# Kernel optimization log

Hardware: AMD Instinct MI355X
Metric: run time of the kernel (lower is better)

## Reference

```python
import jax, jax.numpy as jnp
import numpy as np

DIM = 128
POS_HID = 32
ATTN_HID = 2 * DIM
K = 16
B, N = 4, 4096


def setup_inputs() -> dict:
    key = jax.random.key(0)
    ks = jax.random.split(key, 16)
    s = lambda fan_in: 1.0 / np.sqrt(fan_in)
    inp = {
        "x": jax.random.normal(ks[0], (B, N, DIM), dtype=jnp.float32),
        "pos": jax.random.uniform(ks[1], (B, N, 3), dtype=jnp.float32),
        # linear projections (stored as (in, out); y = x @ W)
        "Wq": jax.random.uniform(ks[2], (DIM, DIM), minval=-s(DIM), maxval=s(DIM)),
        "Wk": jax.random.uniform(ks[3], (DIM, DIM), minval=-s(DIM), maxval=s(DIM)),
        "Wv": jax.random.uniform(ks[4], (DIM, DIM), minval=-s(DIM), maxval=s(DIM)),
        # pos_mlp: 3 -> POS_HID -> DIM
        "p_w1": jax.random.uniform(ks[5], (3, POS_HID), minval=-s(3), maxval=s(3)),
        "p_b1": jax.random.uniform(ks[6], (POS_HID,), minval=-s(3), maxval=s(3)),
        "p_w2": jax.random.uniform(ks[7], (POS_HID, DIM), minval=-s(POS_HID), maxval=s(POS_HID)),
        "p_b2": jax.random.uniform(ks[8], (DIM,), minval=-s(POS_HID), maxval=s(POS_HID)),
        # attn_mlp: DIM -> ATTN_HID -> DIM
        "a_w1": jax.random.uniform(ks[9], (DIM, ATTN_HID), minval=-s(DIM), maxval=s(DIM)),
        "a_b1": jax.random.uniform(ks[10], (ATTN_HID,), minval=-s(DIM), maxval=s(DIM)),
        "a_w2": jax.random.uniform(ks[11], (ATTN_HID, DIM), minval=-s(ATTN_HID), maxval=s(ATTN_HID)),
        "a_b2": jax.random.uniform(ks[12], (DIM,), minval=-s(ATTN_HID), maxval=s(ATTN_HID)),
    }
    return inp


def reference(x, pos, Wq, Wk, Wv, p_w1, p_b1, p_w2, p_b2, a_w1, a_b1, a_w2, a_b2):
    # brute-force kNN: (B, N, N) squared distances, take K smallest
    dists = jnp.sum((pos[:, :, None, :] - pos[:, None, :, :]) ** 2, axis=-1)
    _, knn_idx = jax.lax.top_k(-dists, K)                      # (B, N, K)

    gather = jax.vmap(lambda tbl, idx: tbl[idx])               # (N, C)[ (N,K) ] -> (N,K,C)
    knn_xyz = gather(pos, knn_idx)                              # (B, N, K, 3)

    q = x @ Wq                                                  # (B, N, D)
    k = gather(x @ Wk, knn_idx)                                 # (B, N, K, D)
    v = gather(x @ Wv, knn_idx)                                 # (B, N, K, D)

    rel = pos[:, :, None, :] - knn_xyz                          # (B, N, K, 3)
    pos_enc = jax.nn.relu(rel @ p_w1 + p_b1) @ p_w2 + p_b2      # (B, N, K, D)

    h = q[:, :, None, :] - k + pos_enc                          # (B, N, K, D)
    attn = jax.nn.relu(h @ a_w1 + a_b1) @ a_w2 + a_b2           # (B, N, K, D)
    attn = jax.nn.softmax(attn / np.sqrt(DIM), axis=-2)         # softmax over K

    agg = jnp.einsum("bnkd,bnkd->bnd", attn, v + pos_enc)       # (B, N, D)
    return agg
```

## Files before the change

### kernel.cpp

```cpp
#include <hip/hip_runtime.h>
#include <hip/hip_bf16.h>

#define B_   4
#define N_   4096
#define D_   128
#define PH_  32
#define AH_  256
#define K_   16
#define BN_  (B_*N_)

#define S2_  16
#define SC2_ (N_ / S2_)

typedef __attribute__((ext_vector_type(8))) short short8;
typedef __attribute__((ext_vector_type(4))) float f32x4;

__device__ inline float f4c(const float4& v, int i) {
  return i == 0 ? v.x : i == 1 ? v.y : i == 2 ? v.z : v.w;
}

__device__ inline unsigned short f2bf(float f) {
  unsigned u = __float_as_uint(f);
  unsigned r = u + 0x7fffu + ((u >> 16) & 1u);
  return (unsigned short)(r >> 16);
}

__device__ inline unsigned short f2bfn(float f) {
  __hip_bfloat16 h = __float2bfloat16(f);
  return *reinterpret_cast<unsigned short*>(&h);
}

__device__ inline float bf2f(unsigned short u) {
  return __uint_as_float((unsigned)u << 16);
}

__global__ __launch_bounds__(256) void wshuf_kernel(
    const float* __restrict__ a_w1, const float* __restrict__ a_w2,
    const float* __restrict__ p_w2,
    const float* __restrict__ Wq, const float* __restrict__ Wk, const float* __restrict__ Wv,
    unsigned short* __restrict__ W1f, unsigned short* __restrict__ W2f,
    unsigned short* __restrict__ p2f,
    unsigned short* __restrict__ Wqf, unsigned short* __restrict__ Wkf,
    unsigned short* __restrict__ Wvf)
{
  int tid = blockIdx.x * blockDim.x + threadIdx.x;
  for (int f = tid; f < 4096; f += blockDim.x * gridDim.x) {
    int lane = f & 63, g = lane >> 4, c = lane & 15;
    {
      int nt = f >> 8, kc = (f >> 6) & 3;
      unsigned short o[8];
      #pragma unroll
      for (int j = 0; j < 8; ++j)
        o[j] = f2bf(a_w1[(size_t)(32 * kc + 8 * g + j) * 256 + 16 * nt + c]);
      #pragma unroll
      for (int j = 0; j < 8; ++j) W1f[(size_t)f * 8 + j] = o[j];
    }
    {
      int nt = f >> 9, kc = (f >> 6) & 7;
      unsigned short o[8];
      #pragma unroll
      for (int j = 0; j < 8; ++j)
        o[j] = f2bf(a_w2[(size_t)(32 * kc + 8 * g + j) * 128 + 16 * nt + c]);
      #pragma unroll
      for (int j = 0; j < 8; ++j) W2f[(size_t)f * 8 + j] = o[j];
    }
    if (f < 512) {
      int nt = f >> 6;
      unsigned short o[8];
      #pragma unroll
      for (int j = 0; j < 8; ++j)
        o[j] = f2bf(p_w2[(size_t)(8 * g + j) * 128 + 16 * nt + c]);
      #pragma unroll
      for (int j = 0; j < 8; ++j) p2f[(size_t)f * 8 + j] = o[j];
    }
    if (f < 2048) {
      int nt = f >> 8, kc = (f >> 6) & 3;
      unsigned short oq[8], ok[8], ov[8];
      #pragma unroll
      for (int j = 0; j < 8; ++j) {
        size_t src = (size_t)(32 * kc + 8 * g + j) * 128 + 16 * nt + c;
        oq[j] = f2bf(Wq[src]);
        ok[j] = f2bf(Wk[src]);
        ov[j] = f2bf(Wv[src]);
      }
      #pragma unroll
      for (int j = 0; j < 8; ++j) {
        Wqf[(size_t)f * 8 + j] = oq[j];
        Wkf[(size_t)f * 8 + j] = ok[j];
        Wvf[(size_t)f * 8 + j] = ov[j];
      }
    }
  }
}

__global__ __launch_bounds__(256) void qkv_mfma_kernel(
    const float* __restrict__ x,
    const unsigned short* __restrict__ Wqf, const unsigned short* __restrict__ Wkf,
    const unsigned short* __restrict__ Wvf,
    float* __restrict__ xq, float* __restrict__ xk, float* __restrict__ xv)
{
  const int w = threadIdx.x >> 6, lane = threadIdx.x & 63;
  const int g = lane >> 4, c = lane & 15;
  const int r0 = (blockIdx.x * 4 + w) * 16;

  short8 xa[4];
  const float* xrow = x + (size_t)(r0 + c) * 128;
  #pragma unroll
  for (int kc = 0; kc < 4; ++kc) {
    const int d0 = 32 * kc + 8 * g;
    float4 a4 = *(const float4*)(xrow + d0);
    float4 b4 = *(const float4*)(xrow + d0 + 4);
    #pragma unroll
    for (int j = 0; j < 8; ++j) {
      float vv = j < 4 ? f4c(a4, j) : f4c(b4, j - 4);
      xa[kc][j] = (short)f2bfn(vv);
    }
  }

  const unsigned short* Ws[3] = {Wqf, Wkf, Wvf};
  float* outs[3] = {xq, xk, xv};
  const f32x4 zero4 = {0.f, 0.f, 0.f, 0.f};

  #pragma unroll
  for (int m = 0; m < 3; ++m) {
    f32x4 acc[8];
    #pragma unroll
    for (int i = 0; i < 8; ++i) acc[i] = zero4;
    #pragma unroll
    for (int nt = 0; nt < 8; ++nt) {
      #pragma unroll
      for (int kc = 0; kc < 4; ++kc) {
        short8 bf = *(const short8*)(Ws[m] + ((size_t)(nt * 4 + kc) * 64 + lane) * 8);
        acc[nt] = __builtin_amdgcn_mfma_f32_16x16x32_bf16(xa[kc], bf, acc[nt], 0, 0, 0);
      }
    }
    #pragma unroll
    for (int nt = 0; nt < 8; ++nt)
      #pragma unroll
      for (int r = 0; r < 4; ++r)
        outs[m][(size_t)(r0 + 4 * g + r) * 128 + nt * 16 + c] = acc[nt][r];
  }
}

__global__ __launch_bounds__(256) void knn_sel_kernel(const float* __restrict__ pos,
                                                      float* __restrict__ part)
{
  __shared__ float4 sh[SC2_];
  const int tid = threadIdx.x;
  const int q = blockIdx.x * 256 + tid;
  const int sp = blockIdx.y;
  const int b = q >> 12, i = q & (N_ - 1);
  const float* __restrict__ pb = pos + (size_t)b * N_ * 3;
  const int j0 = sp * SC2_;

  for (int e = tid; e < SC2_; e += 256) {
    const float* src = pb + (size_t)(j0 + e) * 3;
    sh[e] = make_float4(src[0], src[1], src[2], 0.f);
  }
  const float qx = pb[i * 3 + 0], qy = pb[i * 3 + 1], qz = pb[i * 3 + 2];
  __syncthreads();

  float c[16];
  #pragma unroll
  for (int s = 0; s < 16; ++s) c[s] = __int_as_float(0x7f800000);

  #pragma unroll 4
  for (int j = 0; j < SC2_; ++j) {
    float4 pt = sh[j];
    float dx = qx - pt.x;
    float dy = qy - pt.y;
    float dz = qz - pt.z;
    float d2 = __fadd_rn(__fadd_rn(__fmul_rn(dx, dx), __fmul_rn(dy, dy)), __fmul_rn(dz, dz));
    #pragma unroll
    for (int s = 15; s >= 1; --s) c[s] = __builtin_amdgcn_fmed3f(c[s - 1], c[s], d2);
    c[0] = fminf(c[0], d2);
  }

  float* dst = part + ((size_t)sp * BN_ + q) * 16;
  #pragma unroll
  for (int s = 0; s < 16; ++s) dst[s] = c[s];
}

__global__ __launch_bounds__(256) void knn_thresh_kernel(const float* __restrict__ part,
                                                         float* __restrict__ d16,
                                                         int* __restrict__ cnt,
                                                         int* __restrict__ tcnt)
{
  const int w = threadIdx.x >> 6, lane = threadIdx.x & 63;
  const int gg = lane >> 4, s = lane & 15;
  const int q = blockIdx.x * 16 + w * 4 + gg;

  float v[16];
  const float* src = part + ((size_t)s * BN_ + q) * 16;
  #pragma unroll
  for (int t = 0; t < 16; ++t) v[t] = src[t];

  float mn = v[0];
  #pragma unroll
  for (int step = 0; step < 16; ++step) {
    mn = v[0];
    mn = fminf(mn, __shfl_xor(mn, 1, 64));
    mn = fminf(mn, __shfl_xor(mn, 2, 64));
    mn = fminf(mn, __shfl_xor(mn, 4, 64));
    mn = fminf(mn, __shfl_xor(mn, 8, 64));
    if (step == 15) break;
    unsigned long long bal = __ballot(v[0] == mn);
    unsigned grp = (unsigned)((bal >> (16 * gg)) & 0xffffu);
    bool adv = (s == (__ffs(grp) - 1));
    #pragma unroll
    for (int t = 0; t < 15; ++t) v[t] = adv ? v[t + 1] : v[t];
    v[15] = adv ? __int_as_float(0x7f800000) : v[15];
  }
  if (s == 0) { d16[q] = mn; cnt[q] = 0; tcnt[q] = 0; }
}

__global__ __launch_bounds__(256) void knn_emit_kernel(const float* __restrict__ pos,
                                                       const float* __restrict__ d16,
                                                       int* __restrict__ knn,
                                                       int* __restrict__ cnt,
                                                       int* __restrict__ tcnt,
                                                       int* __restrict__ tied)
{
  __shared__ float4 sh[SC2_];
  const int tid = threadIdx.x;
  const int q = blockIdx.x * 256 + tid;
  const int sp = blockIdx.y;
  const int b = q >> 12, i = q & (N_ - 1);
  const float* __restrict__ pb = pos + (size_t)b * N_ * 3;
  const int j0 = sp * SC2_;

  for (int e = tid; e < SC2_; e += 256) {
    const float* src = pb + (size_t)(j0 + e) * 3;
    sh[e] = make_float4(src[0], src[1], src[2], 0.f);
  }
  const float qx = pb[i * 3 + 0], qy = pb[i * 3 + 1], qz = pb[i * 3 + 2];
  const float thr = d16[q];
  __syncthreads();

  for (int j = 0; j < SC2_; ++j) {
    float4 pt = sh[j];
    float dx = qx - pt.x;
    float dy = qy - pt.y;
    float dz = qz - pt.z;
    float d2 = __fadd_rn(__fadd_rn(__fmul_rn(dx, dx), __fmul_rn(dy, dy)), __fmul_rn(dz, dz));
    if (d2 < thr) {
      int p = atomicAdd(&cnt[q], 1);
      knn[(size_t)q * 16 + p] = j0 + j;
    } else if (d2 == thr) {
      int p = atomicAdd(&tcnt[q], 1);
      if (p < 16) tied[(size_t)q * 16 + p] = j0 + j;
    }
  }
}

__global__ __launch_bounds__(256) void knn_fix_kernel(const int* __restrict__ cnt,
                                                      const int* __restrict__ tcnt,
                                                      const int* __restrict__ tied,
                                                      int* __restrict__ knn)
{
  const int q = blockIdx.x * 256 + threadIdx.x;
  const int c_lt = cnt[q];
  int tn = tcnt[q]; if (tn > 16) tn = 16;

  int a[16];
  #pragma unroll
  for (int s = 0; s < 16; ++s) a[s] = (s < tn) ? tied[(size_t)q * 16 + s] : 0x7fffffff;

  #pragma unroll
  for (int pass = 0; pass < 15; ++pass) {
    #pragma unroll
    for (int s = 0; s < 15; ++s) {
      int lo = min(a[s], a[s + 1]);
      int hi = max(a[s], a[s + 1]);
      a[s] = lo; a[s + 1] = hi;
    }
  }

  const int need = 16 - c_lt;
  #pragma unroll
  for (int s = 0; s < 16; ++s)
    if (s < need) knn[(size_t)q * 16 + c_lt + s] = a[s];
}

__global__ __launch_bounds__(256, 3) void fused_mlp_kernel(
    const float* __restrict__ pos,
    const float* __restrict__ xq, const float* __restrict__ xk, const float* __restrict__ xv,
    const int* __restrict__ knn,
    const float* __restrict__ p_w1, const float* __restrict__ p_b1,
    const unsigned short* __restrict__ p2f, const float* __restrict__ p_b2,
    const unsigned short* __restrict__ W1f, const unsigned short* __restrict__ W2f,
    const float* __restrict__ a_b1, const float* __restrict__ a_b2,
    float* __restrict__ out)
{
  __shared__ unsigned short tile[4][16][136];

  const int w = threadIdx.x >> 6, lane = threadIdx.x & 63;
  const int g = lane >> 4, c = lane & 15;
  const size_t p = (size_t)blockIdx.x * 4 + w;
  const int b = (int)(p >> 12);

  const int idx_r = knn[p * 16 + c];
  int idx4[4];
  #pragma unroll
  for (int r = 0; r < 4; ++r) idx4[r] = knn[p * 16 + 4 * g + r];

  const float* vb = xv + (size_t)b * N_ * 128;
  float vreg[8][4];
  #pragma unroll
  for (int r = 0; r < 4; ++r) {
    const float* vrow = vb + (size_t)idx4[r] * 128;
    #pragma unroll
    for (int nt = 0; nt < 8; ++nt) vreg[nt][r] = vrow[nt * 16 + c];
  }

  const float qx = pos[p * 3 + 0], qy = pos[p * 3 + 1], qz = pos[p * 3 + 2];
  const float* pn = pos + ((size_t)b * N_ + idx_r) * 3;
  const float rx = qx - pn[0], ry = qy - pn[1], rz = qz - pn[2];

  short8 hid;
  #pragma unroll
  for (int j = 0; j < 8; ++j) {
    int hh = 8 * g + j;
    float a = p_b1[hh];
    a = fmaf(rx, p_w1[0 * PH_ + hh], a);
    a = fmaf(ry, p_w1[1 * PH_ + hh], a);
    a = fmaf(rz, p_w1[2 * PH_ + hh], a);
    a = fmaxf(a, 0.f);
    hid[j] = (short)f2bfn(a);
  }

  f32x4 pe8[8];
  const f32x4 zero4 = {0.f, 0.f, 0.f, 0.f};
  #pragma unroll
  for (int nt = 0; nt < 8; ++nt) {
    short8 bf = *(const short8*)(p2f + ((size_t)nt * 64 + lane) * 8);
    pe8[nt] = __builtin_amdgcn_mfma_f32_16x16x32_bf16(hid, bf, zero4, 0, 0, 0);
  }
  #pragma unroll
  for (int nt = 0; nt < 8; ++nt) {
    float b2v = p_b2[nt * 16 + c];
    #pragma unroll
    for (int r = 0; r < 4; ++r) {
      pe8[nt][r] += b2v;
      tile[w][g * 4 + r][nt * 16 + c] = f2bfn(pe8[nt][r]);
    }
  }

  short8 ha[4];
  const float* qb = xq + p * 128;
  const float* kb = xk + ((size_t)b * N_ + idx_r) * 128;
  #pragma unroll
  for (int kc = 0; kc < 4; ++kc) {
    const int d0 = 32 * kc + 8 * g;
    float4 q4a = *(const float4*)(qb + d0);
    float4 q4b = *(const float4*)(qb + d0 + 4);
    float4 k4a = *(const float4*)(kb + d0);
    float4 k4b = *(const float4*)(kb + d0 + 4);
    short8 pv = *(const short8*)&tile[w][c][d0];
    #pragma unroll
    for (int j = 0; j < 8; ++j) {
      float qv = j < 4 ? f4c(q4a, j) : f4c(q4b, j - 4);
      float kv = j < 4 ? f4c(k4a, j) : f4c(k4b, j - 4);
      float h = qv - kv + bf2f((unsigned short)pv[j]);
      ha[kc][j] = (short)f2bfn(h);
    }
  }

  unsigned vpe_pk[8][2];
  #pragma unroll
  for (int nt = 0; nt < 8; ++nt) {
    unsigned short e0 = f2bfn(pe8[nt][0] + vreg[nt][0]);
    unsigned short e1 = f2bfn(pe8[nt][1] + vreg[nt][1]);
    unsigned short e2 = f2bfn(pe8[nt][2] + vreg[nt][2]);
    unsigned short e3 = f2bfn(pe8[nt][3] + vreg[nt][3]);
    vpe_pk[nt][0] = (unsigned)e0 | ((unsigned)e1 << 16);
    vpe_pk[nt][1] = (unsigned)e2 | ((unsigned)e3 << 16);
  }

  f32x4 acc2[8];
  #pragma unroll
  for (int i = 0; i < 8; ++i) acc2[i] = zero4;

  #pragma unroll
  for (int h = 0; h < 2; ++h) {
    #pragma unroll
    for (int qq = 0; qq < 2; ++qq) {
      f32x4 acc1[4];
      #pragma unroll
      for (int i = 0; i < 4; ++i) acc1[i] = zero4;

      #pragma unroll
      for (int ntl = 0; ntl < 4; ++ntl) {
        const unsigned short* wb = W1f + (size_t)(h * 8 + qq * 4 + ntl) * 2048 + (size_t)lane * 8;
        #pragma unroll
        for (int kc = 0; kc < 4; ++kc) {
          short8 bf = *(const short8*)(wb + (size_t)kc * 512);
          acc1[ntl] = __builtin_amdgcn_mfma_f32_16x16x32_bf16(ha[kc], bf, acc1[ntl], 0, 0, 0);
        }
      }
      #pragma unroll
      for (int ntl = 0; ntl < 4; ++ntl) {
        float b1v = a_b1[(h * 8 + qq * 4 + ntl) * 16 + c];
        #pragma unroll
        for (int r = 0; r < 4; ++r) {
          float vv = acc1[ntl][r] + b1v;
          vv = fmaxf(vv, 0.f);
          tile[w][g * 4 + r][(qq * 4 + ntl) * 16 + c] = f2bfn(vv);
        }
      }
      #pragma unroll
      for (int k2 = 0; k2 < 2; ++k2) {
        const int kc2 = qq * 2 + k2;
        short8 a2 = *(const short8*)&tile[w][c][kc2 * 32 + g * 8];
        const unsigned short* w2b = W2f + (size_t)(h * 4 + kc2) * 512 + (size_t)lane * 8;
        #pragma unroll
        for (int nt2 = 0; nt2 < 8; ++nt2) {
          short8 b2f = *(const short8*)(w2b + (size_t)nt2 * 4096);
          acc2[nt2] = __builtin_amdgcn_mfma_f32_16x16x32_bf16(a2, b2f, acc2[nt2], 0, 0, 0);
        }
      }
    }
  }

  const float scale = 0.08838834764831845f;
  #pragma unroll
  for (int nt2 = 0; nt2 < 8; ++nt2) {
    float b2v = a_b2[nt2 * 16 + c];
    float l0 = acc2[nt2][0] + b2v;
    float l1 = acc2[nt2][1] + b2v;
    float l2 = acc2[nt2][2] + b2v;
    float l3 = acc2[nt2][3] + b2v;
    float mx = fmaxf(fmaxf(l0, l1), fmaxf(l2, l3));
    mx = fmaxf(mx, __shfl_xor(mx, 16, 64));
    mx = fmaxf(mx, __shfl_xor(mx, 32, 64));
    float e0 = expf((l0 - mx) * scale);
    float e1 = expf((l1 - mx) * scale);
    float e2 = expf((l2 - mx) * scale);
    float e3 = expf((l3 - mx) * scale);
    float s = e0 + e1 + e2 + e3;
    s += __shfl_xor(s, 16, 64);
    s += __shfl_xor(s, 32, 64);
    float inv = 1.f / s;
    float v0 = bf2f((unsigned short)(vpe_pk[nt2][0] & 0xffff));
    float v1 = bf2f((unsigned short)(vpe_pk[nt2][0] >> 16));
    float v2 = bf2f((unsigned short)(vpe_pk[nt2][1] & 0xffff));
    float v3 = bf2f((unsigned short)(vpe_pk[nt2][1] >> 16));
    float ac = (e0 * v0 + e1 * v1 + e2 * v2 + e3 * v3) * inv;
    ac += __shfl_xor(ac, 16, 64);
    ac += __shfl_xor(ac, 32, 64);
    if (g == 0) out[p * 128 + nt2 * 16 + c] = ac;
  }
}

extern "C" void kernel_launch(void* const* d_in, const int* in_sizes, int n_in,
                              void* d_out, int out_size, void* d_ws, size_t ws_size,
                              hipStream_t stream)
{
  const float* x    = (const float*)d_in[0];
  const float* pos  = (const float*)d_in[1];
  const float* Wq   = (const float*)d_in[2];
  const float* Wk   = (const float*)d_in[3];
  const float* Wv   = (const float*)d_in[4];
  const float* p_w1 = (const float*)d_in[5];
  const float* p_b1 = (const float*)d_in[6];
  const float* p_w2 = (const float*)d_in[7];
  const float* p_b2 = (const float*)d_in[8];
  const float* a_w1 = (const float*)d_in[9];
  const float* a_b1 = (const float*)d_in[10];
  const float* a_w2 = (const float*)d_in[11];
  const float* a_b2 = (const float*)d_in[12];
  float* out = (float*)d_out;

  float* xq = (float*)d_ws;
  float* xk = xq + (size_t)BN_ * 128;
  float* xv = xk + (size_t)BN_ * 128;
  int*   knn = (int*)(xv + (size_t)BN_ * 128);
  unsigned short* W1f = (unsigned short*)(knn + (size_t)BN_ * 16);
  unsigned short* W2f = W1f + 32768;
  unsigned short* p2f = W2f + 32768;
  unsigned short* Wqf = p2f + 4096;
  unsigned short* Wkf = Wqf + 16384;
  unsigned short* Wvf = Wkf + 16384;
  float* part = (float*)(Wvf + 16384);
  float* d16  = part + (size_t)S2_ * BN_ * 16;
  int* cnt    = (int*)(d16 + BN_);
  int* tcnt   = cnt + BN_;
  int* tied   = tcnt + BN_;

  wshuf_kernel<<<16, 256, 0, stream>>>(a_w1, a_w2, p_w2, Wq, Wk, Wv,
                                       W1f, W2f, p2f, Wqf, Wkf, Wvf);
  qkv_mfma_kernel<<<BN_ / 64, 256, 0, stream>>>(x, Wqf, Wkf, Wvf, xq, xk, xv);
  knn_sel_kernel<<<dim3(BN_ / 256, S2_), 256, 0, stream>>>(pos, part);
  knn_thresh_kernel<<<BN_ / 16, 256, 0, stream>>>(part, d16, cnt, tcnt);
  knn_emit_kernel<<<dim3(BN_ / 256, S2_), 256, 0, stream>>>(pos, d16, knn, cnt, tcnt, tied);
  knn_fix_kernel<<<BN_ / 256, 256, 0, stream>>>(cnt, tcnt, tied, knn);
  fused_mlp_kernel<<<BN_ / 4, 256, 0, stream>>>(pos, xq, xk, xv, knn,
                                                p_w1, p_b1, p2f, p_b2,
                                                W1f, W2f, a_b1, a_b2, out);
}
```

Baseline: 279.2 us.

## Split QKV projection across grid and pack pos-enc to cut MLP register pressure

```diff
diff --git a/kernel.cpp b/kernel.cpp
--- a/kernel.cpp
+++ b/kernel.cpp
@@ -102,6 +102,7 @@
   const int w = threadIdx.x >> 6, lane = threadIdx.x & 63;
   const int g = lane >> 4, c = lane & 15;
   const int r0 = (blockIdx.x * 4 + w) * 16;
+  const int m = blockIdx.y >> 1, nth = blockIdx.y & 1;
 
   short8 xa[4];
   const float* xrow = x + (size_t)(r0 + c) * 128;
@@ -117,28 +118,22 @@
     }
   }
 
-  const unsigned short* Ws[3] = {Wqf, Wkf, Wvf};
-  float* outs[3] = {xq, xk, xv};
+  const unsigned short* Wm = m == 0 ? Wqf : (m == 1 ? Wkf : Wvf);
+  float* outm = m == 0 ? xq : (m == 1 ? xk : xv);
   const f32x4 zero4 = {0.f, 0.f, 0.f, 0.f};
 
   #pragma unroll
-  for (int m = 0; m < 3; ++m) {
-    f32x4 acc[8];
-    #pragma unroll
-    for (int i = 0; i < 8; ++i) acc[i] = zero4;
-    #pragma unroll
-    for (int nt = 0; nt < 8; ++nt) {
-      #pragma unroll
-      for (int kc = 0; kc < 4; ++kc) {
-        short8 bf = *(const short8*)(Ws[m] + ((size_t)(nt * 4 + kc) * 64 + lane) * 8);
-        acc[nt] = __builtin_amdgcn_mfma_f32_16x16x32_bf16(xa[kc], bf, acc[nt], 0, 0, 0);
-      }
-    }
-    #pragma unroll
-    for (int nt = 0; nt < 8; ++nt)
-      #pragma unroll
-      for (int r = 0; r < 4; ++r)
-        outs[m][(size_t)(r0 + 4 * g + r) * 128 + nt * 16 + c] = acc[nt][r];
+  for (int nt = 0; nt < 4; ++nt) {
+    const int ntg = nth * 4 + nt;
+    f32x4 acc = zero4;
+    #pragma unroll
+    for (int kc = 0; kc < 4; ++kc) {
+      short8 bf = *(const short8*)(Wm + ((size_t)(ntg * 4 + kc) * 64 + lane) * 8);
+      acc = __builtin_amdgcn_mfma_f32_16x16x32_bf16(xa[kc], bf, acc, 0, 0, 0);
+    }
+    #pragma unroll
+    for (int r = 0; r < 4; ++r)
+      outm[(size_t)(r0 + 4 * g + r) * 128 + ntg * 16 + c] = acc[r];
   }
 }
 
@@ -282,7 +277,7 @@
     if (s < need) knn[(size_t)q * 16 + c_lt + s] = a[s];
 }
 
-__global__ __launch_bounds__(256, 3) void fused_mlp_kernel(
+__global__ __launch_bounds__(256, 4) void fused_mlp_kernel(
     const float* __restrict__ pos,
     const float* __restrict__ xq, const float* __restrict__ xk, const float* __restrict__ xv,
     const int* __restrict__ knn,
@@ -329,21 +324,23 @@
     hid[j] = (short)f2bfn(a);
   }
 
-  f32x4 pe8[8];
   const f32x4 zero4 = {0.f, 0.f, 0.f, 0.f};
+  unsigned pe_pk[8][2];
   #pragma unroll
   for (int nt = 0; nt < 8; ++nt) {
     short8 bf = *(const short8*)(p2f + ((size_t)nt * 64 + lane) * 8);
-    pe8[nt] = __builtin_amdgcn_mfma_f32_16x16x32_bf16(hid, bf, zero4, 0, 0, 0);
-  }
-  #pragma unroll
-  for (int nt = 0; nt < 8; ++nt) {
+    f32x4 pe4 = __builtin_amdgcn_mfma_f32_16x16x32_bf16(hid, bf, zero4, 0, 0, 0);
     float b2v = p_b2[nt * 16 + c];
-    #pragma unroll
-    for (int r = 0; r < 4; ++r) {
-      pe8[nt][r] += b2v;
-      tile[w][g * 4 + r][nt * 16 + c] = f2bfn(pe8[nt][r]);
-    }
+    unsigned short e0 = f2bfn(pe4[0] + b2v);
+    unsigned short e1 = f2bfn(pe4[1] + b2v);
+    unsigned short e2 = f2bfn(pe4[2] + b2v);
+    unsigned short e3 = f2bfn(pe4[3] + b2v);
+    pe_pk[nt][0] = (unsigned)e0 | ((unsigned)e1 << 16);
+    pe_pk[nt][1] = (unsigned)e2 | ((unsigned)e3 << 16);
+    tile[w][g * 4 + 0][nt * 16 + c] = e0;
+    tile[w][g * 4 + 1][nt * 16 + c] = e1;
+    tile[w][g * 4 + 2][nt * 16 + c] = e2;
+    tile[w][g * 4 + 3][nt * 16 + c] = e3;
   }
 
   short8 ha[4];
@@ -369,10 +366,10 @@
   unsigned vpe_pk[8][2];
   #pragma unroll
   for (int nt = 0; nt < 8; ++nt) {
-    unsigned short e0 = f2bfn(pe8[nt][0] + vreg[nt][0]);
-    unsigned short e1 = f2bfn(pe8[nt][1] + vreg[nt][1]);
-    unsigned short e2 = f2bfn(pe8[nt][2] + vreg[nt][2]);
-    unsigned short e3 = f2bfn(pe8[nt][3] + vreg[nt][3]);
+    unsigned short e0 = f2bfn(vreg[nt][0] + bf2f((unsigned short)(pe_pk[nt][0] & 0xffff)));
+    unsigned short e1 = f2bfn(vreg[nt][1] + bf2f((unsigned short)(pe_pk[nt][0] >> 16)));
+    unsigned short e2 = f2bfn(vreg[nt][2] + bf2f((unsigned short)(pe_pk[nt][1] & 0xffff)));
+    unsigned short e3 = f2bfn(vreg[nt][3] + bf2f((unsigned short)(pe_pk[nt][1] >> 16)));
     vpe_pk[nt][0] = (unsigned)e0 | ((unsigned)e1 << 16);
     vpe_pk[nt][1] = (unsigned)e2 | ((unsigned)e3 << 16);
   }
@@ -489,7 +486,7 @@
 
   wshuf_kernel<<<16, 256, 0, stream>>>(a_w1, a_w2, p_w2, Wq, Wk, Wv,
                                        W1f, W2f, p2f, Wqf, Wkf, Wvf);
-  qkv_mfma_kernel<<<BN_ / 64, 256, 0, stream>>>(x, Wqf, Wkf, Wvf, xq, xk, xv);
+  qkv_mfma_kernel<<<dim3(BN_ / 64, 6), 256, 0, stream>>>(x, Wqf, Wkf, Wvf, xq, xk, xv);
   knn_sel_kernel<<<dim3(BN_ / 256, S2_), 256, 0, stream>>>(pos, part);
   knn_thresh_kernel<<<BN_ / 16, 256, 0, stream>>>(part, d16, cnt, tcnt);
   knn_emit_kernel<<<dim3(BN_ / 256, S2_), 256, 0, stream>>>(pos, d16, knn, cnt, tcnt, tied);
```

New measurement: 298.3 us. 6.9% more time.
